# Optimization experiments

Hardware: AMD Instinct MI355X
Metric: run time of the kernel (lower is better)

The kernel has to match this reference:

```python
import jax, jax.numpy as jnp
import numpy as np

N, C, C_OUT, E = 50000, 128, 256, 600000


def setup_inputs() -> dict:
    key = jax.random.key(0)
    k1, k2, k3, k4, k5 = jax.random.split(key, 5)
    x = jax.random.normal(k1, (N, C), dtype=jnp.float32)
    edge_index = jax.random.randint(k2, (2, E), 0, N, dtype=jnp.int64)
    # torch Linear(2C -> C_OUT): weight [out, in], bias [out]
    bound = 1.0 / np.sqrt(2 * C)
    W = jax.random.uniform(k3, (C_OUT, 2 * C), dtype=jnp.float32, minval=-bound, maxval=bound)
    b = jax.random.uniform(k4, (C_OUT,), dtype=jnp.float32, minval=-bound, maxval=bound)
    return {"x": x, "edge_index": edge_index, "W": W, "b": b}


def reference(x, edge_index, W, b):
    src, dst = edge_index[0], edge_index[1]
    # gather - subtract: relative features per edge [E, C]
    rel = x[src] - x[dst]
    # scatter-max into destination nodes; empty segments -> 0 (torch_scatter fill)
    x_j = jax.ops.segment_max(rel, dst, num_segments=N)
    x_j = jnp.where(jnp.isfinite(x_j), x_j, 0.0)
    # concat + Linear + ReLU (MLP([2C, C_OUT], act='relu'))
    h = jnp.concatenate([x, x_j], axis=1)  # [N, 2C]
    out = h @ W.T + b
    return jax.nn.relu(out)
```

## Files before the change

### kernel.cpp

```cpp
#include <hip/hip_runtime.h>

#define NNODES 50000
#define CIN    128
#define COUT   256
#define KTOT   256

typedef float  f32x4  __attribute__((ext_vector_type(4)));
typedef short  bf16x8 __attribute__((ext_vector_type(8)));

#define GLOAD16(gptr, lptr) __builtin_amdgcn_global_load_lds(                      \
    (const __attribute__((address_space(1))) void*)(gptr),                         \
    (__attribute__((address_space(3))) void*)(lptr), 16, 0, 0)

__device__ __forceinline__ unsigned short f2bf(float f) {
    union { float f; unsigned int u; } v; v.f = f;
    unsigned int r = v.u + 0x7FFFu + ((v.u >> 16) & 1u);
    return (unsigned short)(r >> 16);
}

__global__ void zero_cnt(int* __restrict__ cnt, int n) {
    int i = blockIdx.x * blockDim.x + threadIdx.x;
    if (i < n) cnt[i] = 0;
}

__global__ void hist_kernel(const int* __restrict__ dst, int* __restrict__ cnt, int E) {
    int i = blockIdx.x * blockDim.x + threadIdx.x;
    if (i < E) atomicAdd(&cnt[dst[i]], 1);
}

__global__ void scan_partial(const int* __restrict__ cnt, int* __restrict__ partial, int n) {
    __shared__ int s[256];
    int tid = threadIdx.x;
    int i = blockIdx.x * 256 + tid;
    s[tid] = (i < n) ? cnt[i] : 0;
    __syncthreads();
    for (int off = 128; off > 0; off >>= 1) {
        if (tid < off) s[tid] += s[tid + off];
        __syncthreads();
    }
    if (tid == 0) partial[blockIdx.x] = s[0];
}

__global__ void scan_root(int* __restrict__ partial, int np) {
    __shared__ int s[256];
    int tid = threadIdx.x;
    int v = (tid < np) ? partial[tid] : 0;
    s[tid] = v;
    __syncthreads();
    for (int off = 1; off < 256; off <<= 1) {
        int t = (tid >= off) ? s[tid - off] : 0;
        __syncthreads();
        s[tid] += t;
        __syncthreads();
    }
    if (tid < np) partial[tid] = s[tid] - v;
}

__global__ void scan_final(const int* __restrict__ cnt, const int* __restrict__ partial,
                           int* __restrict__ row_start, int n) {
    __shared__ int s[256];
    int tid = threadIdx.x;
    int i = blockIdx.x * 256 + tid;
    int v = (i < n) ? cnt[i] : 0;
    s[tid] = v;
    __syncthreads();
    for (int off = 1; off < 256; off <<= 1) {
        int t = (tid >= off) ? s[tid - off] : 0;
        __syncthreads();
        s[tid] += t;
        __syncthreads();
    }
    int incl = s[tid];
    int base = partial[blockIdx.x];
    if (i < n) row_start[i] = base + incl - v;
    if (i == n - 1) row_start[n] = base + incl;
}

__global__ void scatter_kernel(const int* __restrict__ src, const int* __restrict__ dst,
                               const int* __restrict__ row_start, int* __restrict__ cnt,
                               int* __restrict__ sorted_src, int E) {
    int i = blockIdx.x * blockDim.x + threadIdx.x;
    if (i < E) {
        int d = dst[i];
        int pos = atomicSub(&cnt[d], 1) - 1;
        sorted_src[row_start[d] + pos] = src[i];
    }
}

__device__ __forceinline__ float2 fmax2(float2 a, float2 b) {
    return make_float2(fmaxf(a.x, b.x), fmaxf(a.y, b.y));
}

__global__ __launch_bounds__(256)
void gather_max_kernel(const float* __restrict__ x,
                       const int* __restrict__ row_start,
                       const int* __restrict__ sorted_src,
                       unsigned short* __restrict__ xcat) {
    int wid  = (blockIdx.x * blockDim.x + threadIdx.x) >> 6;
    int lane = threadIdx.x & 63;
    if (wid >= NNODES) return;

    int start = row_start[wid];
    int end   = row_start[wid + 1];

    const float NI = __int_as_float(0xFF800000u);
    float2 m0 = make_float2(NI, NI), m1 = m0, m2 = m0, m3 = m0;

    int t = start;
    for (; t + 4 <= end; t += 4) {
        int s0 = sorted_src[t + 0];
        int s1 = sorted_src[t + 1];
        int s2 = sorted_src[t + 2];
        int s3 = sorted_src[t + 3];
        float2 v0 = ((const float2*)(x + (size_t)s0 * CIN))[lane];
        float2 v1 = ((const float2*)(x + (size_t)s1 * CIN))[lane];
        float2 v2 = ((const float2*)(x + (size_t)s2 * CIN))[lane];
        float2 v3 = ((const float2*)(x + (size_t)s3 * CIN))[lane];
        m0 = fmax2(m0, v0); m1 = fmax2(m1, v1);
        m2 = fmax2(m2, v2); m3 = fmax2(m3, v3);
    }
    for (; t < end; ++t) {
        int s = sorted_src[t];
        m0 = fmax2(m0, ((const float2*)(x + (size_t)s * CIN))[lane]);
    }
    float2 mx = fmax2(fmax2(m0, m1), fmax2(m2, m3));

    float2 xv = ((const float2*)(x + (size_t)wid * CIN))[lane];
    bool nonempty = (end > start);
    float2 o;
    o.x = nonempty ? mx.x - xv.x : 0.0f;
    o.y = nonempty ? mx.y - xv.y : 0.0f;

    ushort2 px = make_ushort2(f2bf(xv.x), f2bf(xv.y));
    ushort2 pj = make_ushort2(f2bf(o.x),  f2bf(o.y));
    *((ushort2*)(xcat + (size_t)wid * KTOT + lane * 2))        = px;
    *((ushort2*)(xcat + (size_t)wid * KTOT + CIN + lane * 2))  = pj;
}

__global__ void convert_w(const float* __restrict__ W, unsigned short* __restrict__ Wbf) {
    int i = blockIdx.x * blockDim.x + threadIdx.x;
    float4 v = ((const float4*)W)[i];
    ushort4 p = make_ushort4(f2bf(v.x), f2bf(v.y), f2bf(v.z), f2bf(v.w));
    *((ushort4*)(Wbf + (size_t)i * 4)) = p;
}

__global__ __launch_bounds__(256, 3)
void mfma_gemm(const unsigned short* __restrict__ xcat,
               const unsigned short* __restrict__ Wbf,
               const float* __restrict__ bias,
               float* __restrict__ out) {
    __shared__ unsigned short As[2][128][32];
    __shared__ unsigned short Bs[2][128][32];

    const int M = NNODES;
    const int bx = blockIdx.x;
    const int nb = bx & 1;
    const int mb = bx >> 1;
    const int m0 = mb * 128, n0 = nb * 128;

    const int tid  = threadIdx.x;
    const int lane = tid & 63;
    const int wid  = tid >> 6;
    const int wm   = wid >> 1;
    const int wn   = wid & 1;

    f32x4 acc[4][4] = {};

    auto stage = [&](int b, int kt) {
#pragma unroll
        for (int j = 0; j < 2; ++j) {
            int u    = j * 256 + tid;
            int row  = u >> 2;
            int kseg = (u & 3) * 8;
            int grow = m0 + row; if (grow > M - 1) grow = M - 1;
            GLOAD16(xcat + (size_t)grow * KTOT + kt + kseg, &As[b][row][kseg]);
            GLOAD16(Wbf  + (size_t)(n0 + row) * KTOT + kt + kseg, &Bs[b][row][kseg]);
        }
    };

    stage(0, 0);
    __syncthreads();

    const int l15 = lane & 15;
    const int kh  = (lane >> 4) * 8;

#pragma unroll
    for (int t = 0; t < 8; ++t) {
        int b = t & 1;
        if (t < 7) stage(b ^ 1, (t + 1) * 32);

        bf16x8 af[4], bfr[4];
#pragma unroll
        for (int m = 0; m < 4; ++m)
            af[m] = *(const bf16x8*)&As[b][wm * 64 + m * 16 + l15][kh];
#pragma unroll
        for (int n = 0; n < 4; ++n)
            bfr[n] = *(const bf16x8*)&Bs[b][wn * 64 + n * 16 + l15][kh];
#pragma unroll
        for (int m = 0; m < 4; ++m)
#pragma unroll
            for (int n = 0; n < 4; ++n)
                acc[m][n] = __builtin_amdgcn_mfma_f32_16x16x32_bf16(af[m], bfr[n], acc[m][n], 0, 0, 0);

        __syncthreads();
    }

#pragma unroll
    for (int n = 0; n < 4; ++n) {
        int col = n0 + wn * 64 + n * 16 + l15;
        float bv = bias[col];
#pragma unroll
        for (int m = 0; m < 4; ++m) {
            int r0 = m0 + wm * 64 + m * 16 + ((lane >> 4) << 2);
            f32x4 a = acc[m][n];
#pragma unroll
            for (int r = 0; r < 4; ++r) {
                int rr = r0 + r;
                if (rr < M) out[(size_t)rr * COUT + col] = fmaxf(a[r] + bv, 0.0f);
            }
        }
    }
}

extern "C" void kernel_launch(void* const* d_in, const int* in_sizes, int n_in,
                              void* d_out, int out_size, void* d_ws, size_t ws_size,
                              hipStream_t stream) {
    const float* x  = (const float*)d_in[0];
    const int*   ei = (const int*)d_in[1];
    const float* W  = (const float*)d_in[2];
    const float* b  = (const float*)d_in[3];
    float*       out = (float*)d_out;

    const int E = in_sizes[1] / 2;
    const int* src = ei;
    const int* dst = ei + E;

    unsigned short* xcat      = (unsigned short*)d_ws;
    unsigned short* Wbf       = xcat + (size_t)NNODES * KTOT;
    int*            cnt       = (int*)(Wbf + COUT * KTOT);
    int*            row_start = cnt + NNODES;
    int*            sorted_src= row_start + (NNODES + 1);
    int*            partial   = sorted_src + E;

    const int NB_N = (NNODES + 255) / 256;
    const int NB_E = (E + 255) / 256;

    convert_w<<<64, 256, 0, stream>>>(W, Wbf);
    zero_cnt<<<NB_N, 256, 0, stream>>>(cnt, NNODES);
    hist_kernel<<<NB_E, 256, 0, stream>>>(dst, cnt, E);
    scan_partial<<<NB_N, 256, 0, stream>>>(cnt, partial, NNODES);
    scan_root<<<1, 256, 0, stream>>>(partial, NB_N);
    scan_final<<<NB_N, 256, 0, stream>>>(cnt, partial, row_start, NNODES);
    scatter_kernel<<<NB_E, 256, 0, stream>>>(src, dst, row_start, cnt, sorted_src, E);
    gather_max_kernel<<<(NNODES * 64 + 255) / 256, 256, 0, stream>>>(x, row_start, sorted_src, xcat);
    mfma_gemm<<<((NNODES + 127) / 128) * 2, 256, 0, stream>>>(xcat, Wbf, b, out);
}
```

Measured before the change: 218.0 us.

## Fuse prep kernels, single-pass scan, gather bf16 x, widen GEMM N tile

Merges the weight conversion, count zeroing and a new x-to-bf16 conversion into one prep kernel. The three-kernel scan becomes a single 1024-thread block. The gather-max now reads bf16 rows from xcat instead of fp32 x, which halves gather bytes, and it writes only the x_j half. The GEMM changes from 128x128 tiles to 64x256 tiles so A is loaded once per row block. The trade-offs are bf16 rounding before the subtraction, which changes accuracy, and a scan serialised on one workgroup.

```diff
diff --git a/kernel.cpp b/kernel.cpp
--- a/kernel.cpp
+++ b/kernel.cpp
@@ -17,10 +17,33 @@
     unsigned int r = v.u + 0x7FFFu + ((v.u >> 16) & 1u);
     return (unsigned short)(r >> 16);
 }
-
-__global__ void zero_cnt(int* __restrict__ cnt, int n) {
-    int i = blockIdx.x * blockDim.x + threadIdx.x;
-    if (i < n) cnt[i] = 0;
+__device__ __forceinline__ float bf2f(unsigned short u) {
+    return __uint_as_float((unsigned int)u << 16);
+}
+
+#define PREP_X   1600000
+#define PREP_C   1650000
+#define PREP_W   1666384
+
+__global__ __launch_bounds__(256)
+void prep_kernel(const float* __restrict__ x, const float* __restrict__ W,
+                 unsigned short* __restrict__ xcat, unsigned short* __restrict__ Wbf,
+                 int* __restrict__ cnt) {
+    int g = blockIdx.x * 256 + threadIdx.x;
+    if (g < PREP_X) {
+        float4 v = ((const float4*)x)[g];
+        int row = g >> 5;
+        int col = (g & 31) * 4;
+        *(ushort4*)(xcat + (size_t)row * KTOT + col) =
+            make_ushort4(f2bf(v.x), f2bf(v.y), f2bf(v.z), f2bf(v.w));
+    } else if (g < PREP_C) {
+        cnt[g - PREP_X] = 0;
+    } else if (g < PREP_W) {
+        int i = g - PREP_C;
+        float4 v = ((const float4*)W)[i];
+        *(ushort4*)(Wbf + (size_t)i * 4) =
+            make_ushort4(f2bf(v.x), f2bf(v.y), f2bf(v.z), f2bf(v.w));
+    }
 }
 
 __global__ void hist_kernel(const int* __restrict__ dst, int* __restrict__ cnt, int E) {
@@ -28,52 +51,41 @@
     if (i < E) atomicAdd(&cnt[dst[i]], 1);
 }
 
-__global__ void scan_partial(const int* __restrict__ cnt, int* __restrict__ partial, int n) {
-    __shared__ int s[256];
-    int tid = threadIdx.x;
-    int i = blockIdx.x * 256 + tid;
-    s[tid] = (i < n) ? cnt[i] : 0;
-    __syncthreads();
-    for (int off = 128; off > 0; off >>= 1) {
-        if (tid < off) s[tid] += s[tid + off];
+__global__ __launch_bounds__(1024)
+void scan_onepass(const int* __restrict__ cnt, int* __restrict__ row_start) {
+    __shared__ int tile[4096];
+    __shared__ int tsum[1024];
+    const int tid = threadIdx.x;
+    int carry = 0;
+
+    for (int c0 = 0; c0 < NNODES; c0 += 4096) {
+#pragma unroll
+        for (int j = 0; j < 4; ++j) {
+            int idx = c0 + j * 1024 + tid;
+            tile[j * 1024 + tid] = (idx < NNODES) ? cnt[idx] : 0;
+        }
         __syncthreads();
-    }
-    if (tid == 0) partial[blockIdx.x] = s[0];
-}
-
-__global__ void scan_root(int* __restrict__ partial, int np) {
-    __shared__ int s[256];
-    int tid = threadIdx.x;
-    int v = (tid < np) ? partial[tid] : 0;
-    s[tid] = v;
-    __syncthreads();
-    for (int off = 1; off < 256; off <<= 1) {
-        int t = (tid >= off) ? s[tid - off] : 0;
+        int a0 = tile[tid * 4 + 0], a1 = tile[tid * 4 + 1];
+        int a2 = tile[tid * 4 + 2], a3 = tile[tid * 4 + 3];
+        int s = a0 + a1 + a2 + a3;
+        tsum[tid] = s;
         __syncthreads();
-        s[tid] += t;
-        __syncthreads();
-    }
-    if (tid < np) partial[tid] = s[tid] - v;
-}
-
-__global__ void scan_final(const int* __restrict__ cnt, const int* __restrict__ partial,
-                           int* __restrict__ row_start, int n) {
-    __shared__ int s[256];
-    int tid = threadIdx.x;
-    int i = blockIdx.x * 256 + tid;
-    int v = (i < n) ? cnt[i] : 0;
-    s[tid] = v;
-    __syncthreads();
-    for (int off = 1; off < 256; off <<= 1) {
-        int t = (tid >= off) ? s[tid - off] : 0;
-        __syncthreads();
-        s[tid] += t;
-        __syncthreads();
-    }
-    int incl = s[tid];
-    int base = partial[blockIdx.x];
-    if (i < n) row_start[i] = base + incl - v;
-    if (i == n - 1) row_start[n] = base + incl;
+        for (int off = 1; off < 1024; off <<= 1) {
+            int t = (tid >= off) ? tsum[tid - off] : 0;
+            __syncthreads();
+            tsum[tid] += t;
+            __syncthreads();
+        }
+        int excl = tsum[tid] - s + carry;
+        int chunktot = tsum[1023];
+        int base = c0 + tid * 4;
+        if (base < NNODES) {
+            *(int4*)&row_start[base] = make_int4(excl, excl + a0, excl + a0 + a1,
+                                                 excl + a0 + a1 + a2);
+        }
+        carry += chunktot;
+    }
+    if (tid == 0) row_start[NNODES] = carry;
 }
 
 __global__ void scatter_kernel(const int* __restrict__ src, const int* __restrict__ dst,
@@ -112,16 +124,19 @@
         int s1 = sorted_src[t + 1];
         int s2 = sorted_src[t + 2];
         int s3 = sorted_src[t + 3];
-        float2 v0 = ((const float2*)(x + (size_t)s0 * CIN))[lane];
-        float2 v1 = ((const float2*)(x + (size_t)s1 * CIN))[lane];
-        float2 v2 = ((const float2*)(x + (size_t)s2 * CIN))[lane];
-        float2 v3 = ((const float2*)(x + (size_t)s3 * CIN))[lane];
-        m0 = fmax2(m0, v0); m1 = fmax2(m1, v1);
-        m2 = fmax2(m2, v2); m3 = fmax2(m3, v3);
+        ushort2 u0 = *(const ushort2*)(xcat + (size_t)s0 * KTOT + lane * 2);
+        ushort2 u1 = *(const ushort2*)(xcat + (size_t)s1 * KTOT + lane * 2);
+        ushort2 u2 = *(const ushort2*)(xcat + (size_t)s2 * KTOT + lane * 2);
+        ushort2 u3 = *(const ushort2*)(xcat + (size_t)s3 * KTOT + lane * 2);
+        m0 = fmax2(m0, make_float2(bf2f(u0.x), bf2f(u0.y)));
+        m1 = fmax2(m1, make_float2(bf2f(u1.x), bf2f(u1.y)));
+        m2 = fmax2(m2, make_float2(bf2f(u2.x), bf2f(u2.y)));
+        m3 = fmax2(m3, make_float2(bf2f(u3.x), bf2f(u3.y)));
     }
     for (; t < end; ++t) {
         int s = sorted_src[t];
-        m0 = fmax2(m0, ((const float2*)(x + (size_t)s * CIN))[lane]);
+        ushort2 u = *(const ushort2*)(xcat + (size_t)s * KTOT + lane * 2);
+        m0 = fmax2(m0, make_float2(bf2f(u.x), bf2f(u.y)));
     }
     float2 mx = fmax2(fmax2(m0, m1), fmax2(m2, m3));
 
@@ -130,18 +145,8 @@
     float2 o;
     o.x = nonempty ? mx.x - xv.x : 0.0f;
     o.y = nonempty ? mx.y - xv.y : 0.0f;
-
-    ushort2 px = make_ushort2(f2bf(xv.x), f2bf(xv.y));
-    ushort2 pj = make_ushort2(f2bf(o.x),  f2bf(o.y));
-    *((ushort2*)(xcat + (size_t)wid * KTOT + lane * 2))        = px;
-    *((ushort2*)(xcat + (size_t)wid * KTOT + CIN + lane * 2))  = pj;
-}
-
-__global__ void convert_w(const float* __restrict__ W, unsigned short* __restrict__ Wbf) {
-    int i = blockIdx.x * blockDim.x + threadIdx.x;
-    float4 v = ((const float4*)W)[i];
-    ushort4 p = make_ushort4(f2bf(v.x), f2bf(v.y), f2bf(v.z), f2bf(v.w));
-    *((ushort4*)(Wbf + (size_t)i * 4)) = p;
+    *((ushort2*)(xcat + (size_t)wid * KTOT + CIN + lane * 2)) =
+        make_ushort2(f2bf(o.x), f2bf(o.y));
 }
 
 __global__ __launch_bounds__(256, 3)
@@ -149,32 +154,31 @@
                const unsigned short* __restrict__ Wbf,
                const float* __restrict__ bias,
                float* __restrict__ out) {
-    __shared__ unsigned short As[2][128][32];
-    __shared__ unsigned short Bs[2][128][32];
+    __shared__ unsigned short As[2][64][32];
+    __shared__ unsigned short Bs[2][256][32];
 
     const int M = NNODES;
-    const int bx = blockIdx.x;
-    const int nb = bx & 1;
-    const int mb = bx >> 1;
-    const int m0 = mb * 128, n0 = nb * 128;
+    const int m0 = blockIdx.x * 64;
 
     const int tid  = threadIdx.x;
     const int lane = tid & 63;
     const int wid  = tid >> 6;
-    const int wm   = wid >> 1;
-    const int wn   = wid & 1;
 
     f32x4 acc[4][4] = {};
 
     auto stage = [&](int b, int kt) {
-#pragma unroll
-        for (int j = 0; j < 2; ++j) {
+        {
+            int row  = tid >> 2;
+            int kseg = (tid & 3) * 8;
+            int grow = m0 + row; if (grow > M - 1) grow = M - 1;
+            GLOAD16(xcat + (size_t)grow * KTOT + kt + kseg, &As[b][row][kseg]);
+        }
+#pragma unroll
+        for (int j = 0; j < 4; ++j) {
             int u    = j * 256 + tid;
             int row  = u >> 2;
             int kseg = (u & 3) * 8;
-            int grow = m0 + row; if (grow > M - 1) grow = M - 1;
-            GLOAD16(xcat + (size_t)grow * KTOT + kt + kseg, &As[b][row][kseg]);
-            GLOAD16(Wbf  + (size_t)(n0 + row) * KTOT + kt + kseg, &Bs[b][row][kseg]);
+            GLOAD16(Wbf + (size_t)row * KTOT + kt + kseg, &Bs[b][row][kseg]);
         }
     };
 
@@ -192,10 +196,10 @@
         bf16x8 af[4], bfr[4];
 #pragma unroll
         for (int m = 0; m < 4; ++m)
-            af[m] = *(const bf16x8*)&As[b][wm * 64 + m * 16 + l15][kh];
+            af[m] = *(const bf16x8*)&As[b][m * 16 + l15][kh];
 #pragma unroll
         for (int n = 0; n < 4; ++n)
-            bfr[n] = *(const bf16x8*)&Bs[b][wn * 64 + n * 16 + l15][kh];
+            bfr[n] = *(const bf16x8*)&Bs[b][wid * 64 + n * 16 + l15][kh];
 #pragma unroll
         for (int m = 0; m < 4; ++m)
 #pragma unroll
@@ -207,11 +211,11 @@
 
 #pragma unroll
     for (int n = 0; n < 4; ++n) {
-        int col = n0 + wn * 64 + n * 16 + l15;
+        int col = wid * 64 + n * 16 + l15;
         float bv = bias[col];
 #pragma unroll
         for (int m = 0; m < 4; ++m) {
-            int r0 = m0 + wm * 64 + m * 16 + ((lane >> 4) << 2);
+            int r0 = m0 + m * 16 + ((lane >> 4) << 2);
             f32x4 a = acc[m][n];
 #pragma unroll
             for (int r = 0; r < 4; ++r) {
@@ -235,23 +239,18 @@
     const int* src = ei;
     const int* dst = ei + E;
 
-    unsigned short* xcat      = (unsigned short*)d_ws;
-    unsigned short* Wbf       = xcat + (size_t)NNODES * KTOT;
-    int*            cnt       = (int*)(Wbf + COUT * KTOT);
-    int*            row_start = cnt + NNODES;
-    int*            sorted_src= row_start + (NNODES + 1);
-    int*            partial   = sorted_src + E;
-
-    const int NB_N = (NNODES + 255) / 256;
+    unsigned short* xcat       = (unsigned short*)d_ws;
+    unsigned short* Wbf        = xcat + (size_t)NNODES * KTOT;
+    int*            cnt        = (int*)(Wbf + COUT * KTOT);
+    int*            row_start  = cnt + NNODES;
+    int*            sorted_src = row_start + (NNODES + 1);
+
     const int NB_E = (E + 255) / 256;
 
-    convert_w<<<64, 256, 0, stream>>>(W, Wbf);
-    zero_cnt<<<NB_N, 256, 0, stream>>>(cnt, NNODES);
+    prep_kernel<<<(PREP_W + 255) / 256, 256, 0, stream>>>(x, W, xcat, Wbf, cnt);
     hist_kernel<<<NB_E, 256, 0, stream>>>(dst, cnt, E);
-    scan_partial<<<NB_N, 256, 0, stream>>>(cnt, partial, NNODES);
-    scan_root<<<1, 256, 0, stream>>>(partial, NB_N);
-    scan_final<<<NB_N, 256, 0, stream>>>(cnt, partial, row_start, NNODES);
+    scan_onepass<<<1, 1024, 0, stream>>>(cnt, row_start);
     scatter_kernel<<<NB_E, 256, 0, stream>>>(src, dst, row_start, cnt, sorted_src, E);
     gather_max_kernel<<<(NNODES * 64 + 255) / 256, 256, 0, stream>>>(x, row_start, sorted_src, xcat);
-    mfma_gemm<<<((NNODES + 127) / 128) * 2, 256, 0, stream>>>(xcat, Wbf, b, out);
-}
+    mfma_gemm<<<(NNODES + 63) / 64, 256, 0, stream>>>(xcat, Wbf, b, out);
+}
```

Result: slower. 234.9 us (+7.7%).
